# Kernel tuning notes

Measured on AMD Instinct MI355X. Metric: run time of the kernel, lower is better.

Reference implementation:

```python
import jax, jax.numpy as jnp
import numpy as np

GROUP_SIZE = 128

def _dequant(q, s, zp):
    # q: [out, in] int values in [0, 2^bits); s, zp: [out, in//GROUP_SIZE]
    out_dim, in_dim = q.shape
    g = s.shape[1]
    qf = q.reshape(out_dim, g, GROUP_SIZE).astype(s.dtype)
    zf = zp[:, :, None].astype(s.dtype)
    return ((qf - zf) * s[:, :, None]).reshape(out_dim, in_dim)

def setup_inputs() -> dict:
    key = jax.random.key(0)
    ks = jax.random.split(key, 10)
    H, I = 4096, 11008
    T = 64  # decode-like token count -> weight-traffic bound
    gH, gI = H // GROUP_SIZE, I // GROUP_SIZE  # 32, 86
    x = jax.random.normal(ks[0], (T, H), dtype=jnp.float32)
    q1 = jax.random.randint(ks[1], (I, H), 0, 16, dtype=jnp.int32)
    s1 = jax.random.uniform(ks[2], (I, gH), dtype=jnp.float32) * 0.05
    zp1 = jax.random.randint(ks[3], (I, gH), 0, 16, dtype=jnp.int32)
    q3 = jax.random.randint(ks[4], (I, H), 0, 16, dtype=jnp.int32)
    s3 = jax.random.uniform(ks[5], (I, gH), dtype=jnp.float32) * 0.05
    zp3 = jax.random.randint(ks[6], (I, gH), 0, 16, dtype=jnp.int32)
    q2 = jax.random.randint(ks[7], (H, I), 0, 16, dtype=jnp.int32)
    s2 = jax.random.uniform(ks[8], (H, gI), dtype=jnp.float32) * 0.05
    zp2 = jax.random.randint(ks[9], (H, gI), 0, 16, dtype=jnp.int32)
    return {"x": x, "q1": q1, "s1": s1, "zp1": zp1, "q3": q3, "s3": s3,
            "zp3": zp3, "q2": q2, "s2": s2, "zp2": zp2}

def reference(x, q1, s1, zp1, q3, s3, zp3, q2, s2, zp2):
    w1 = _dequant(q1, s1, zp1)  # [I, H]
    w3 = _dequant(q3, s3, zp3)  # [I, H]
    w2 = _dequant(q2, s2, zp2)  # [H, I]
    x1 = x @ w1.T               # [T, I]
    x3 = x @ w3.T               # [T, I]
    x13 = jax.nn.silu(x1) * x3  # OPMX.silu(x1, x3): silu gate times up-proj
    return x13 @ w2.T           # [T, H]
```

## Files before the change

### kernel.cpp

```cpp
#include <hip/hip_runtime.h>
#include <hip/hip_fp16.h>

typedef _Float16 f16;
typedef f16 f16x8 __attribute__((ext_vector_type(8)));
typedef float f32x4 __attribute__((ext_vector_type(4)));

constexpr int T = 64;
constexpr int H = 4096;
constexpr int I = 11008;
constexpr int GH = 32;
constexpr int GI = 86;

__device__ __forceinline__ void gll16(const void* g, void* l) {
    __builtin_amdgcn_global_load_lds(
        (const __attribute__((address_space(1))) unsigned int*)g,
        (__attribute__((address_space(3))) unsigned int*)l, 16, 0, 0);
}

__device__ __forceinline__ f16x8 dq8v(int4 a, int4 b, float sv, float zv) {
    f16x8 r;
    auto p0 = __builtin_amdgcn_cvt_pkrtz((float)a.x * sv - zv, (float)a.y * sv - zv);
    auto p1 = __builtin_amdgcn_cvt_pkrtz((float)a.z * sv - zv, (float)a.w * sv - zv);
    auto p2 = __builtin_amdgcn_cvt_pkrtz((float)b.x * sv - zv, (float)b.y * sv - zv);
    auto p3 = __builtin_amdgcn_cvt_pkrtz((float)b.z * sv - zv, (float)b.w * sv - zv);
    r[0] = p0[0]; r[1] = p0[1]; r[2] = p1[0]; r[3] = p1[1];
    r[4] = p2[0]; r[5] = p2[1]; r[6] = p3[0]; r[7] = p3[1];
    return r;
}

__global__ __launch_bounds__(256) void k_cvt(const float* __restrict__ x,
                                             f16* __restrict__ xp) {
    int C = blockIdx.x * 256 + threadIdx.x;
    int w = C >> 8, m = (C >> 2) & 63, hi = C & 3;
    const float* src = x + (size_t)m * H + w * 32 + hi * 8;
    float4 a = *(const float4*)src;
    float4 b = *(const float4*)(src + 4);
    f16x8 o;
    o[0] = (f16)a.x; o[1] = (f16)a.y; o[2] = (f16)a.z; o[3] = (f16)a.w;
    o[4] = (f16)b.x; o[5] = (f16)b.y; o[6] = (f16)b.z; o[7] = (f16)b.w;
    *(f16x8*)(xp + (size_t)C * 8) = o;
}

template<int KDIM>
__device__ __forceinline__ void stage_tile(const int* __restrict__ q, int R0, int g,
                                           int* buf) {
    const int t = threadIdx.x;
    #pragma unroll
    for (int k4 = 0; k4 < 8; ++k4) {
        int P = t + k4 * 256;
        int row = P >> 5, c = P & 31, cs = c ^ (row & 7);
        size_t gb = (size_t)(R0 + row) * ((size_t)KDIM * 4) + (size_t)g * 512 + cs * 16;
        gll16((const char*)q + gb, (void*)&buf[((t >> 6) * 64 + k4 * 256) * 4]);
    }
}

__global__ __launch_bounds__(256, 2) void k_gateup(
    const f16* __restrict__ xp,
    const int* __restrict__ q1, const float* __restrict__ s1, const int* __restrict__ zp1,
    const int* __restrict__ q3, const float* __restrict__ s3, const int* __restrict__ zp3,
    float* __restrict__ part)
{
    __shared__ int tile[2][8192];
    const int t = threadIdx.x;
    const int wv = t >> 6, lane = t & 63, lo = lane & 15, hi = lane >> 4;
    const int R0 = blockIdx.x * 64;
    const int ks = blockIdx.y;
    const int mat = blockIdx.z;
    const int rot = blockIdx.x & 7;
    const int brow = wv * 16 + lo;
    const int grow = R0 + brow;

    const int*   q  = mat ? q3 : q1;
    const float* sm = mat ? s3 : s1;
    const int*   zm = mat ? zp3 : zp1;

    f32x4 acc[4] = {};
    int cur = 0;

    stage_tile<H>(q, R0, ks * 8 + rot, tile[0]);

    for (int gl = 0; gl < 8; ++gl) {
        int g = ks * 8 + ((gl + rot) & 7);
        float sv = sm[(size_t)grow * GH + g];
        float zv = (float)zm[(size_t)grow * GH + g] * sv;

        f16x8 areg[16];
        #pragma unroll
        for (int w = 0; w < 4; ++w)
            #pragma unroll
            for (int mt = 0; mt < 4; ++mt)
                areg[w * 4 + mt] = *(const f16x8*)(xp +
                    ((size_t)(g * 4 + w) * 256 + (mt * 16 + lo) * 4 + hi) * 8);
        asm volatile("" ::: "memory");

        int gn = ks * 8 + (((gl < 7 ? gl + 1 : gl) + rot) & 7);
        stage_tile<H>(q, R0, gn, tile[cur ^ 1]);

        asm volatile("s_waitcnt vmcnt(8)" ::: "memory");
        __syncthreads();

        const char* tb = (const char*)tile[cur];
        #pragma unroll
        for (int w = 0; w < 4; ++w) {
            int cc = (w * 8 + hi * 2) ^ (brow & 7);
            int byte0 = (brow * 32 + cc) * 16;
            int4 b0 = *(const int4*)(tb + byte0);
            int4 b1 = *(const int4*)(tb + (byte0 ^ 16));
            f16x8 bf = dq8v(b0, b1, sv, zv);
            #pragma unroll
            for (int mt = 0; mt < 4; ++mt)
                acc[mt] = __builtin_amdgcn_mfma_f32_16x16x32_f16(areg[w * 4 + mt], bf, acc[mt], 0, 0, 0);
        }
        __syncthreads();
        cur ^= 1;
    }

    float* pb = part + (size_t)(ks * 2 + mat) * T * I;
    #pragma unroll
    for (int mt = 0; mt < 4; ++mt)
        #pragma unroll
        for (int j = 0; j < 4; ++j)
            pb[(size_t)(mt * 16 + hi * 4 + j) * I + R0 + brow] = acc[mt][j];
}

__global__ __launch_bounds__(256) void k_comb(const float* __restrict__ part,
                                              f16* __restrict__ hp) {
    int C = blockIdx.x * 256 + threadIdx.x;
    int w = C >> 8, m = (C >> 2) & 63, hi = C & 3;
    int col = w * 32 + hi * 8;
    float ga[8] = {}, ua[8] = {};
    #pragma unroll
    for (int ks = 0; ks < 4; ++ks) {
        const float* pg = part + ((size_t)(ks * 2 + 0) * T + m) * I + col;
        const float* pu = part + ((size_t)(ks * 2 + 1) * T + m) * I + col;
        float4 g0 = *(const float4*)pg, g1 = *(const float4*)(pg + 4);
        float4 u0 = *(const float4*)pu, u1 = *(const float4*)(pu + 4);
        ga[0] += g0.x; ga[1] += g0.y; ga[2] += g0.z; ga[3] += g0.w;
        ga[4] += g1.x; ga[5] += g1.y; ga[6] += g1.z; ga[7] += g1.w;
        ua[0] += u0.x; ua[1] += u0.y; ua[2] += u0.z; ua[3] += u0.w;
        ua[4] += u1.x; ua[5] += u1.y; ua[6] += u1.z; ua[7] += u1.w;
    }
    f16x8 o;
    #pragma unroll
    for (int j = 0; j < 8; ++j) {
        float gv = ga[j];
        o[j] = (f16)(gv / (1.f + __expf(-gv)) * ua[j]);
    }
    *(f16x8*)(hp + (size_t)C * 8) = o;
}

__global__ __launch_bounds__(256, 2) void k_down(
    const f16* __restrict__ hp,
    const int* __restrict__ q2, const float* __restrict__ s2, const int* __restrict__ zp2,
    float* __restrict__ part2)
{
    __shared__ int tile[2][8192];
    const int t = threadIdx.x;
    const int wv = t >> 6, lane = t & 63, lo = lane & 15, hi = lane >> 4;
    const int R0 = blockIdx.x * 64;
    const int y = blockIdx.y;
    const int g0 = (y * GI) >> 3, g1 = ((y + 1) * GI) >> 3;
    const int cnt = g1 - g0;
    const int rot = blockIdx.x % cnt;
    const int brow = wv * 16 + lo;
    const int grow = R0 + brow;

    f32x4 acc[4] = {};
    int cur = 0;

    stage_tile<I>(q2, R0, g0 + rot, tile[0]);

    for (int gl = 0; gl < cnt; ++gl) {
        int gi = rot + gl;      if (gi >= cnt) gi -= cnt;
        int g = g0 + gi;
        float sv = s2[(size_t)grow * GI + g];
        float zv = (float)zp2[(size_t)grow * GI + g] * sv;

        f16x8 areg[16];
        #pragma unroll
        for (int w = 0; w < 4; ++w)
            #pragma unroll
            for (int mt = 0; mt < 4; ++mt)
                areg[w * 4 + mt] = *(const f16x8*)(hp +
                    ((size_t)(g * 4 + w) * 256 + (mt * 16 + lo) * 4 + hi) * 8);
        asm volatile("" ::: "memory");

        int gj = rot + (gl + 1 < cnt ? gl + 1 : gl);  if (gj >= cnt) gj -= cnt;
        stage_tile<I>(q2, R0, g0 + gj, tile[cur ^ 1]);

        asm volatile("s_waitcnt vmcnt(8)" ::: "memory");
        __syncthreads();

        const char* tb = (const char*)tile[cur];
        #pragma unroll
        for (int w = 0; w < 4; ++w) {
            int cc = (w * 8 + hi * 2) ^ (brow & 7);
            int byte0 = (brow * 32 + cc) * 16;
            int4 b0 = *(const int4*)(tb + byte0);
            int4 b1 = *(const int4*)(tb + (byte0 ^ 16));
            f16x8 bf = dq8v(b0, b1, sv, zv);
            #pragma unroll
            for (int mt = 0; mt < 4; ++mt)
                acc[mt] = __builtin_amdgcn_mfma_f32_16x16x32_f16(areg[w * 4 + mt], bf, acc[mt], 0, 0, 0);
        }
        __syncthreads();
        cur ^= 1;
    }

    float* pb = part2 + (size_t)y * T * H;
    #pragma unroll
    for (int mt = 0; mt < 4; ++mt)
        #pragma unroll
        for (int j = 0; j < 4; ++j)
            pb[(size_t)(mt * 16 + hi * 4 + j) * H + R0 + brow] = acc[mt][j];
}

__global__ __launch_bounds__(256) void k_red(const float* __restrict__ part2,
                                             float* __restrict__ out) {
    int i = (blockIdx.x * 256 + threadIdx.x) * 4;
    float4 s = {0.f, 0.f, 0.f, 0.f};
    #pragma unroll
    for (int y = 0; y < 8; ++y) {
        float4 v = *(const float4*)(part2 + (size_t)y * T * H + i);
        s.x += v.x; s.y += v.y; s.z += v.z; s.w += v.w;
    }
    *(float4*)(out + i) = s;
}

extern "C" void kernel_launch(void* const* d_in, const int* in_sizes, int n_in,
                              void* d_out, int out_size, void* d_ws, size_t ws_size,
                              hipStream_t stream) {
    const float* x   = (const float*)d_in[0];
    const int*   q1  = (const int*)d_in[1];
    const float* s1  = (const float*)d_in[2];
    const int*   zp1 = (const int*)d_in[3];
    const int*   q3  = (const int*)d_in[4];
    const float* s3  = (const float*)d_in[5];
    const int*   zp3 = (const int*)d_in[6];
    const int*   q2  = (const int*)d_in[7];
    const float* s2  = (const float*)d_in[8];
    const int*   zp2 = (const int*)d_in[9];

    char* ws = (char*)d_ws;
    f16*   xp    = (f16*)ws;
    f16*   hp    = (f16*)(ws + 524288);
    float* part  = (float*)(ws + 524288 + 1409024);
    float* part2 = (float*)(ws + 524288 + 1409024 + 22544384);

    k_cvt<<<128, 256, 0, stream>>>(x, xp);
    k_gateup<<<dim3(172, 4, 2), 256, 0, stream>>>(xp, q1, s1, zp1, q3, s3, zp3, part);
    k_comb<<<344, 256, 0, stream>>>(part, hp);
    k_down<<<dim3(64, 8), 256, 0, stream>>>(hp, q2, s2, zp2, part2);
    k_red<<<256, 256, 0, stream>>>(part2, (float*)d_out);
}
```

Baseline: 170.2 us.

## Pack int32 gate/up weights to 4-bit nibbles before the gate-up GEMM

Adds a k_pack kernel that compresses the int32 q1/q3 weights into 4-bit nibbles, eight per 32-bit word, in workspace. k_gateup then loads each block's whole K-slice into shared memory in one shot, dequantizes straight from the nibbles, and reads activations inside the inner loop. The double-buffered prefetch is gone and the occupancy hint rises from 2 to 4 blocks. The packing runs on every call, so the full int32 weights are still read once plus an extra packed write. That may cancel the reduced traffic in the GEMM itself.

```diff
diff --git a/kernel.cpp b/kernel.cpp
--- a/kernel.cpp
+++ b/kernel.cpp
@@ -10,11 +10,42 @@
 constexpr int I = 11008;
 constexpr int GH = 32;
 constexpr int GI = 86;
+constexpr int IH8 = I * H / 8;
 
 __device__ __forceinline__ void gll16(const void* g, void* l) {
     __builtin_amdgcn_global_load_lds(
         (const __attribute__((address_space(1))) unsigned int*)g,
         (__attribute__((address_space(3))) unsigned int*)l, 16, 0, 0);
+}
+
+__global__ __launch_bounds__(256) void k_pack(const int* __restrict__ q,
+                                              unsigned* __restrict__ p, int n_words) {
+    int stride = gridDim.x * 256;
+    for (int w = blockIdx.x * 256 + threadIdx.x; w < n_words; w += stride) {
+        const int* s = q + (size_t)w * 8;
+        int4 a = *(const int4*)s;
+        int4 b = *(const int4*)(s + 4);
+        unsigned v = (unsigned)(a.x & 15) | ((unsigned)(a.y & 15) << 4)
+                   | ((unsigned)(a.z & 15) << 8) | ((unsigned)(a.w & 15) << 12)
+                   | ((unsigned)(b.x & 15) << 16) | ((unsigned)(b.y & 15) << 20)
+                   | ((unsigned)(b.z & 15) << 24) | ((unsigned)(b.w & 15) << 28);
+        p[w] = v;
+    }
+}
+
+__device__ __forceinline__ f16x8 dq8p(unsigned pw, float sv, float zv) {
+    f16x8 r;
+    auto c0 = __builtin_amdgcn_cvt_pkrtz((float)(pw & 15u) * sv - zv,
+                                         (float)((pw >> 4) & 15u) * sv - zv);
+    auto c1 = __builtin_amdgcn_cvt_pkrtz((float)((pw >> 8) & 15u) * sv - zv,
+                                         (float)((pw >> 12) & 15u) * sv - zv);
+    auto c2 = __builtin_amdgcn_cvt_pkrtz((float)((pw >> 16) & 15u) * sv - zv,
+                                         (float)((pw >> 20) & 15u) * sv - zv);
+    auto c3 = __builtin_amdgcn_cvt_pkrtz((float)((pw >> 24) & 15u) * sv - zv,
+                                         (float)(pw >> 28) * sv - zv);
+    r[0] = c0[0]; r[1] = c0[1]; r[2] = c1[0]; r[3] = c1[1];
+    r[4] = c2[0]; r[5] = c2[1]; r[6] = c3[0]; r[7] = c3[1];
+    return r;
 }
 
 __device__ __forceinline__ f16x8 dq8v(int4 a, int4 b, float sv, float zv) {
@@ -41,78 +72,52 @@
     *(f16x8*)(xp + (size_t)C * 8) = o;
 }
 
-template<int KDIM>
-__device__ __forceinline__ void stage_tile(const int* __restrict__ q, int R0, int g,
-                                           int* buf) {
-    const int t = threadIdx.x;
-    #pragma unroll
-    for (int k4 = 0; k4 < 8; ++k4) {
-        int P = t + k4 * 256;
-        int row = P >> 5, c = P & 31, cs = c ^ (row & 7);
-        size_t gb = (size_t)(R0 + row) * ((size_t)KDIM * 4) + (size_t)g * 512 + cs * 16;
-        gll16((const char*)q + gb, (void*)&buf[((t >> 6) * 64 + k4 * 256) * 4]);
-    }
-}
-
-__global__ __launch_bounds__(256, 2) void k_gateup(
+__global__ __launch_bounds__(256, 4) void k_gateup(
     const f16* __restrict__ xp,
-    const int* __restrict__ q1, const float* __restrict__ s1, const int* __restrict__ zp1,
-    const int* __restrict__ q3, const float* __restrict__ s3, const int* __restrict__ zp3,
+    const unsigned* __restrict__ q1p, const float* __restrict__ s1, const int* __restrict__ zp1,
+    const unsigned* __restrict__ q3p, const float* __restrict__ s3, const int* __restrict__ zp3,
     float* __restrict__ part)
 {
-    __shared__ int tile[2][8192];
+    __shared__ unsigned tile[8192];
     const int t = threadIdx.x;
     const int wv = t >> 6, lane = t & 63, lo = lane & 15, hi = lane >> 4;
     const int R0 = blockIdx.x * 64;
     const int ks = blockIdx.y;
     const int mat = blockIdx.z;
-    const int rot = blockIdx.x & 7;
     const int brow = wv * 16 + lo;
     const int grow = R0 + brow;
 
-    const int*   q  = mat ? q3 : q1;
-    const float* sm = mat ? s3 : s1;
-    const int*   zm = mat ? zp3 : zp1;
+    const unsigned* qp = mat ? q3p : q1p;
+    const float*    sm = mat ? s3 : s1;
+    const int*      zm = mat ? zp3 : zp1;
+
+    #pragma unroll
+    for (int k4 = 0; k4 < 8; ++k4) {
+        int P = t + k4 * 256;
+        int row = P >> 5, c = P & 31, cs = c ^ (row & 7);
+        size_t gb = (size_t)(R0 + row) * 2048 + (size_t)ks * 512 + cs * 16;
+        gll16((const char*)qp + gb, (void*)(tile + ((t >> 6) * 64 + k4 * 256) * 4));
+    }
+    asm volatile("s_waitcnt vmcnt(0)" ::: "memory");
+    __syncthreads();
 
     f32x4 acc[4] = {};
-    int cur = 0;
-
-    stage_tile<H>(q, R0, ks * 8 + rot, tile[0]);
-
-    for (int gl = 0; gl < 8; ++gl) {
-        int g = ks * 8 + ((gl + rot) & 7);
-        float sv = sm[(size_t)grow * GH + g];
-        float zv = (float)zm[(size_t)grow * GH + g] * sv;
-
-        f16x8 areg[16];
-        #pragma unroll
-        for (int w = 0; w < 4; ++w)
+
+    for (int g = 0; g < 8; ++g) {
+        int gg = ks * 8 + g;
+        float sv = sm[(size_t)grow * GH + gg];
+        float zv = (float)zm[(size_t)grow * GH + gg] * sv;
+        #pragma unroll
+        for (int w = 0; w < 4; ++w) {
+            unsigned pw = tile[brow * 128 + (((g * 4 + w) ^ (brow & 7)) << 2) + hi];
+            f16x8 bf = dq8p(pw, sv, zv);
             #pragma unroll
-            for (int mt = 0; mt < 4; ++mt)
-                areg[w * 4 + mt] = *(const f16x8*)(xp +
-                    ((size_t)(g * 4 + w) * 256 + (mt * 16 + lo) * 4 + hi) * 8);
-        asm volatile("" ::: "memory");
-
-        int gn = ks * 8 + (((gl < 7 ? gl + 1 : gl) + rot) & 7);
-        stage_tile<H>(q, R0, gn, tile[cur ^ 1]);
-
-        asm volatile("s_waitcnt vmcnt(8)" ::: "memory");
-        __syncthreads();
-
-        const char* tb = (const char*)tile[cur];
-        #pragma unroll
-        for (int w = 0; w < 4; ++w) {
-            int cc = (w * 8 + hi * 2) ^ (brow & 7);
-            int byte0 = (brow * 32 + cc) * 16;
-            int4 b0 = *(const int4*)(tb + byte0);
-            int4 b1 = *(const int4*)(tb + (byte0 ^ 16));
-            f16x8 bf = dq8v(b0, b1, sv, zv);
-            #pragma unroll
-            for (int mt = 0; mt < 4; ++mt)
-                acc[mt] = __builtin_amdgcn_mfma_f32_16x16x32_f16(areg[w * 4 + mt], bf, acc[mt], 0, 0, 0);
+            for (int mt = 0; mt < 4; ++mt) {
+                f16x8 af = *(const f16x8*)(xp +
+                    ((size_t)(gg * 4 + w) * 256 + (mt * 16 + lo) * 4 + hi) * 8);
+                acc[mt] = __builtin_amdgcn_mfma_f32_16x16x32_f16(af, bf, acc[mt], 0, 0, 0);
+            }
         }
-        __syncthreads();
-        cur ^= 1;
     }
 
     float* pb = part + (size_t)(ks * 2 + mat) * T * I;
@@ -147,6 +152,18 @@
         o[j] = (f16)(gv / (1.f + __expf(-gv)) * ua[j]);
     }
     *(f16x8*)(hp + (size_t)C * 8) = o;
+}
+
+__device__ __forceinline__ void stage_tile_q2(const int* __restrict__ q, int R0, int g,
+                                              int* buf) {
+    const int t = threadIdx.x;
+    #pragma unroll
+    for (int k4 = 0; k4 < 8; ++k4) {
+        int P = t + k4 * 256;
+        int row = P >> 5, c = P & 31, cs = c ^ (row & 7);
+        size_t gb = (size_t)(R0 + row) * ((size_t)I * 4) + (size_t)g * 512 + cs * 16;
+        gll16((const char*)q + gb, (void*)&buf[((t >> 6) * 64 + k4 * 256) * 4]);
+    }
 }
 
 __global__ __launch_bounds__(256, 2) void k_down(
@@ -168,7 +185,7 @@
     f32x4 acc[4] = {};
     int cur = 0;
 
-    stage_tile<I>(q2, R0, g0 + rot, tile[0]);
+    stage_tile_q2(q2, R0, g0 + rot, tile[0]);
 
     for (int gl = 0; gl < cnt; ++gl) {
         int gi = rot + gl;      if (gi >= cnt) gi -= cnt;
@@ -186,7 +203,7 @@
         asm volatile("" ::: "memory");
 
         int gj = rot + (gl + 1 < cnt ? gl + 1 : gl);  if (gj >= cnt) gj -= cnt;
-        stage_tile<I>(q2, R0, g0 + gj, tile[cur ^ 1]);
+        stage_tile_q2(q2, R0, g0 + gj, tile[cur ^ 1]);
 
         asm volatile("s_waitcnt vmcnt(8)" ::: "memory");
         __syncthreads();
@@ -242,13 +259,17 @@
     const int*   zp2 = (const int*)d_in[9];
 
     char* ws = (char*)d_ws;
-    f16*   xp    = (f16*)ws;
-    f16*   hp    = (f16*)(ws + 524288);
-    float* part  = (float*)(ws + 524288 + 1409024);
-    float* part2 = (float*)(ws + 524288 + 1409024 + 22544384);
-
+    f16*      xp    = (f16*)ws;
+    f16*      hp    = (f16*)(ws + 524288);
+    unsigned* q1p   = (unsigned*)(ws + 1933312);
+    unsigned* q3p   = (unsigned*)(ws + 24477696);
+    float*    part  = (float*)(ws + 47022080);
+    float*    part2 = (float*)(ws + 1933312);
+
+    k_pack<<<2048, 256, 0, stream>>>(q1, q1p, IH8);
+    k_pack<<<2048, 256, 0, stream>>>(q3, q3p, IH8);
     k_cvt<<<128, 256, 0, stream>>>(x, xp);
-    k_gateup<<<dim3(172, 4, 2), 256, 0, stream>>>(xp, q1, s1, zp1, q3, s3, zp3, part);
+    k_gateup<<<dim3(172, 4, 2), 256, 0, stream>>>(xp, q1p, s1, zp1, q3p, s3, zp3, part);
     k_comb<<<344, 256, 0, stream>>>(part, hp);
     k_down<<<dim3(64, 8), 256, 0, stream>>>(hp, q2, s2, zp2, part2);
     k_red<<<256, 256, 0, stream>>>(part2, (float*)d_out);
```

Result: slower. 211.1 us (+24.0%).
